# Kernel optimization log

Measured on AMD Instinct MI355X. Metric: run time of the kernel, lower is better.

The kernel has to match this reference:

```python
import jax, jax.numpy as jnp
import numpy as np

B, TV, TS, D = 16, 256, 32, 512


def setup_inputs() -> dict:
    key = jax.random.key(0)
    ks = jax.random.split(key, 8)
    return {
        "video_feature": jax.random.normal(ks[0], (B, TV, D), dtype=jnp.float32),
        "video_mask": jnp.ones((B, TV), dtype=jnp.float32),
        "sentence_feature": jax.random.normal(ks[1], (B, TS, D), dtype=jnp.float32),
        "sentence_mask": jnp.ones((B, TS), dtype=jnp.float32),
        "w1": jax.random.normal(ks[2], (D, D), dtype=jnp.float32) * (1.0 / np.sqrt(D)),
        "b1": jax.random.normal(ks[3], (D,), dtype=jnp.float32) * 0.02,
        "w2": jax.random.normal(ks[4], (D, D), dtype=jnp.float32) * (1.0 / np.sqrt(D)),
        "wt": jax.random.normal(ks[5], (D,), dtype=jnp.float32) * (1.0 / np.sqrt(D)),
    }


def reference(video_feature, video_mask, sentence_feature, sentence_mask, w1, b1, w2, wt):
    # tmp1: [B, Tv, D] masked video projection (Linear with bias)
    tmp1 = (jnp.einsum("bvd,ed->bve", video_feature, w1) + b1) * video_mask[:, :, None]
    # tmp2: [B, Ts, D] masked sentence projection (Linear, no bias)
    tmp2 = jnp.einsum("bsd,ed->bse", sentence_feature, w2) * sentence_mask[:, :, None]
    # pairwise mask: [B, Tv, Ts]
    pair_mask = video_mask[:, :, None] * sentence_mask[:, None, :]
    # broadcast-add -> [B, Tv, Ts, D], mask, tanh, reduce with wt -> [B, Tv, Ts]
    tmp = (tmp1[:, :, None, :] + tmp2[:, None, :, :]) * pair_mask[..., None]
    M = jnp.einsum("bvsd,d->bvs", jnp.tanh(tmp), wt)
    return M * pair_mask
```

## Files before the change

### kernel.cpp

```cpp
#include <hip/hip_runtime.h>

#define BB 16
#define TV 256
#define TS 32
#define DD 512

typedef float    floatx4  __attribute__((ext_vector_type(4)));
typedef short    short8   __attribute__((ext_vector_type(8)));
typedef unsigned short ushort8 __attribute__((ext_vector_type(8)));

#define TANH_SCALE 2.885390082f

static __device__ __forceinline__ unsigned short f2bf(float f) {
    unsigned int u = __float_as_uint(f);
    u += 0x7FFFu + ((u >> 16) & 1u);
    return (unsigned short)(u >> 16);
}

__global__ __launch_bounds__(256) void ta_convert(
    const float* __restrict__ video, const float* __restrict__ sent,
    const float* __restrict__ w1,    const float* __restrict__ w2,
    unsigned short* __restrict__ vb, unsigned short* __restrict__ sb,
    unsigned short* __restrict__ w1b, unsigned short* __restrict__ w2b)
{
    const int NV = BB * TV * DD, NS = BB * TS * DD, NW = DD * DD;
    const int base = (blockIdx.x * 256 + threadIdx.x) * 8;
    const float* src; unsigned short* dst; int off;
    if      (base < NV)           { src = video; dst = vb;  off = base; }
    else if (base < NV + NS)      { src = sent;  dst = sb;  off = base - NV; }
    else if (base < NV + NS + NW) { src = w1;    dst = w1b; off = base - NV - NS; }
    else                          { src = w2;    dst = w2b; off = base - NV - NS - NW; }
    const float4 a = *(const float4*)(src + off);
    const float4 b = *(const float4*)(src + off + 4);
    ushort8 o;
    o[0] = f2bf(a.x); o[1] = f2bf(a.y); o[2] = f2bf(a.z); o[3] = f2bf(a.w);
    o[4] = f2bf(b.x); o[5] = f2bf(b.y); o[6] = f2bf(b.z); o[7] = f2bf(b.w);
    *(ushort8*)(dst + off) = o;
}

__global__ __launch_bounds__(256) void ta_mfma_gemm(
    const unsigned short* __restrict__ vb, const unsigned short* __restrict__ w1b,
    const float* __restrict__ b1,          const float* __restrict__ vmask,
    float* __restrict__ tmp1e,
    const unsigned short* __restrict__ sb, const unsigned short* __restrict__ w2b,
    const float* __restrict__ smask,       unsigned short* __restrict__ tmp2h,
    const float* __restrict__ wt,          float* __restrict__ wsum)
{
    const int t = threadIdx.x;

    if (blockIdx.x == 0 && t < 64) {
        float v = 0.f;
        for (int i = t; i < DD; i += 64) v += wt[i];
        for (int off = 32; off; off >>= 1) v += __shfl_down(v, off);
        if (t == 0) wsum[0] = v;
    }

    const bool g2 = (blockIdx.x >= 512);
    const int bid = g2 ? (int)blockIdx.x - 512 : (int)blockIdx.x;
    const unsigned short* __restrict__ A = g2 ? sb    : vb;
    const unsigned short* __restrict__ W = g2 ? w2b   : w1b;
    const float* __restrict__ rm         = g2 ? smask : vmask;
    const int m0 = (g2 ? (bid & 7)  : (bid & 63)) * 64;
    const int n0 = (g2 ? (bid >> 3) : (bid >> 6)) * 64;

    __shared__ unsigned short As[2][4096];
    __shared__ unsigned short Bs[2][4096];

    const int lane = t & 63;
    const int wid  = t >> 6;
    const int wm   = wid >> 1, wn = wid & 1;
    const int lr   = lane & 15, kg = lane >> 4;

    const int r0 = t >> 3,          g0c = (t & 7) ^ (r0 & 7);
    const int r1 = (t + 256) >> 3,  g1c = (t & 7) ^ (r1 & 7);
    const unsigned short* a0p = A + (size_t)(m0 + r0) * DD + g0c * 8;
    const unsigned short* a1p = A + (size_t)(m0 + r1) * DD + g1c * 8;
    const unsigned short* w0p = W + (size_t)(n0 + r0) * DD + g0c * 8;
    const unsigned short* w1p = W + (size_t)(n0 + r1) * DD + g1c * 8;
    const int l0 = t * 8;
    const int l1 = (t + 256) * 8;

#define TA_STAGE(buf, koff) do {                                               \
    __builtin_amdgcn_global_load_lds(                                          \
        (const __attribute__((address_space(1))) void*)(a0p + (koff)),         \
        (__attribute__((address_space(3))) void*)&As[buf][l0], 16, 0, 0);      \
    __builtin_amdgcn_global_load_lds(                                          \
        (const __attribute__((address_space(1))) void*)(a1p + (koff)),         \
        (__attribute__((address_space(3))) void*)&As[buf][l1], 16, 0, 0);      \
    __builtin_amdgcn_global_load_lds(                                          \
        (const __attribute__((address_space(1))) void*)(w0p + (koff)),         \
        (__attribute__((address_space(3))) void*)&Bs[buf][l0], 16, 0, 0);      \
    __builtin_amdgcn_global_load_lds(                                          \
        (const __attribute__((address_space(1))) void*)(w1p + (koff)),         \
        (__attribute__((address_space(3))) void*)&Bs[buf][l1], 16, 0, 0);      \
  } while (0)

    floatx4 acc[2][2] = {};

    const int ml0 = wm * 32 + lr, ml1 = ml0 + 16;
    const int nl0 = wn * 32 + lr, nl1 = nl0 + 16;
    const int sa0 = ml0 * 64, sa1 = ml1 * 64;
    const int sb0 = nl0 * 64, sb1 = nl1 * 64;
    const int xa = ml0 & 7, xb = nl0 & 7;

    TA_STAGE(0, 0);
    __syncthreads();

    int cur = 0;
    for (int step = 0; step < 8; ++step) {
        if (step < 7) TA_STAGE(cur ^ 1, (step + 1) * 64);
#pragma unroll
        for (int kk = 0; kk < 2; ++kk) {
            const int kc = kk * 4 + kg;
            short8 a0 = *(const short8*)&As[cur][sa0 + ((kc ^ xa) << 3)];
            short8 a1 = *(const short8*)&As[cur][sa1 + ((kc ^ xa) << 3)];
            short8 b0 = *(const short8*)&Bs[cur][sb0 + ((kc ^ xb) << 3)];
            short8 b1 = *(const short8*)&Bs[cur][sb1 + ((kc ^ xb) << 3)];
            acc[0][0] = __builtin_amdgcn_mfma_f32_16x16x32_bf16(a0, b0, acc[0][0], 0, 0, 0);
            acc[0][1] = __builtin_amdgcn_mfma_f32_16x16x32_bf16(a0, b1, acc[0][1], 0, 0, 0);
            acc[1][0] = __builtin_amdgcn_mfma_f32_16x16x32_bf16(a1, b0, acc[1][0], 0, 0, 0);
            acc[1][1] = __builtin_amdgcn_mfma_f32_16x16x32_bf16(a1, b1, acc[1][1], 0, 0, 0);
        }
        __syncthreads();
        cur ^= 1;
    }
#undef TA_STAGE

#pragma unroll
    for (int fm = 0; fm < 2; ++fm)
#pragma unroll
        for (int fn = 0; fn < 2; ++fn)
#pragma unroll
            for (int r = 0; r < 4; ++r) {
                const int m = m0 + wm * 32 + fm * 16 + kg * 4 + r;
                const int n = n0 + wn * 32 + fn * 16 + lr;
                const float mk = rm[m] * TANH_SCALE;
                float z = g2 ? (acc[fm][fn][r] * mk)
                             : (acc[fm][fn][r] + b1[n]) * mk;
                z = fminf(fmaxf(z, -30.f), 30.f);
                const float e = __builtin_amdgcn_exp2f(z);
                if (!g2) {
                    tmp1e[(size_t)m * DD + n] = e;
                } else {
                    tmp2h[(size_t)(m >> 5) * 16384 + (size_t)(n >> 1) * 64
                          + (m & 31) * 2 + (n & 1)] = f2bf(e);
                }
            }
}

__global__ __launch_bounds__(512, 4) void ta_tanh_main(
    const float* __restrict__ tmp1e,
    const unsigned short* __restrict__ tmp2h,
    const float* __restrict__ wt,
    const float* __restrict__ wsum,
    const float* __restrict__ vmask,
    const float* __restrict__ smask,
    float* __restrict__ out)
{
    __shared__ unsigned int t2u[8192];
    __shared__ float e1s[8 * DD];
    __shared__ float part[1024];

    const int t  = threadIdx.x;
    const int b  = blockIdx.x >> 5;
    const int v0 = (blockIdx.x & 31) << 3;

    {
        const ushort8* src = (const ushort8*)(tmp2h + (size_t)b * 16384);
        ushort8* dst = (ushort8*)t2u;
#pragma unroll
        for (int i = 0; i < 4; ++i) dst[t + 512 * i] = src[t + 512 * i];
#pragma unroll
        for (int i = 0; i < 2; ++i) {
            const int c = t + 512 * i;
            const int row = c >> 7, col = (c & 127) << 2;
            *(float4*)&e1s[row * DD + col] =
                *(const float4*)&tmp1e[(size_t)(b * TV + v0 + row) * DD + col];
        }
    }
    __syncthreads();

    const int s  = t & 31;
    const int vi = (t >> 5) & 3;
    const int q  = t >> 7;

    const float* __restrict__ e1lo = e1s + vi * DD + q * 128;
    const float* __restrict__ e1hi = e1s + (vi + 4) * DD + q * 128;
    const float* __restrict__ wtp  = wt + q * 128;
    const int ubase = q * 2048 + s;

    floatx4 alo = {0.f, 0.f, 0.f, 0.f};
    floatx4 ahi = {0.f, 0.f, 0.f, 0.f};
#pragma unroll 4
    for (int i = 0; i < 16; ++i) {
        const int ub = ubase + i * 128;
        const unsigned u0 = t2u[ub];
        const unsigned u1 = t2u[ub + 32];
        const unsigned u2 = t2u[ub + 64];
        const unsigned u3 = t2u[ub + 96];
        floatx4 xl0 = *(const floatx4*)(e1lo + i * 8);
        floatx4 xl1 = *(const floatx4*)(e1lo + i * 8 + 4);
        floatx4 xh0 = *(const floatx4*)(e1hi + i * 8);
        floatx4 xh1 = *(const floatx4*)(e1hi + i * 8 + 4);
        floatx4 wa  = *(const floatx4*)(wtp + i * 8);
        floatx4 wb  = *(const floatx4*)(wtp + i * 8 + 4);
        float e2[8] = {
            __uint_as_float(u0 << 16), __uint_as_float(u0 & 0xffff0000u),
            __uint_as_float(u1 << 16), __uint_as_float(u1 & 0xffff0000u),
            __uint_as_float(u2 << 16), __uint_as_float(u2 & 0xffff0000u),
            __uint_as_float(u3 << 16), __uint_as_float(u3 & 0xffff0000u)
        };
#pragma unroll
        for (int j = 0; j < 4; ++j) {
            const float dlo = fmaf(xl0[j], e2[j], 1.f);
            const float dhi = fmaf(xh0[j], e2[j], 1.f);
            const float inv = __builtin_amdgcn_rcpf(dlo * dhi);
            alo[j] = fmaf(wa[j], dhi * inv, alo[j]);
            ahi[j] = fmaf(wa[j], dlo * inv, ahi[j]);
        }
#pragma unroll
        for (int j = 0; j < 4; ++j) {
            const float dlo = fmaf(xl1[j], e2[j + 4], 1.f);
            const float dhi = fmaf(xh1[j], e2[j + 4], 1.f);
            const float inv = __builtin_amdgcn_rcpf(dlo * dhi);
            alo[j] = fmaf(wb[j], dhi * inv, alo[j]);
            ahi[j] = fmaf(wb[j], dlo * inv, ahi[j]);
        }
    }

    part[vi * 128 + s * 4 + q]       = (alo[0] + alo[1]) + (alo[2] + alo[3]);
    part[(vi + 4) * 128 + s * 4 + q] = (ahi[0] + ahi[1]) + (ahi[2] + ahi[3]);
    __syncthreads();

    if (t < 256) {
        const int sv = t >> 5, s2 = t & 31;
        const float4 p4 = *(const float4*)&part[sv * 128 + s2 * 4];
        const float sum = (p4.x + p4.y) + (p4.z + p4.w);
        const int v = v0 + sv;
        const float pm = vmask[b * TV + v] * smask[b * TS + s2];
        out[((size_t)b * TV + v) * TS + s2] = pm * (wsum[0] - 2.f * sum);
    }
}

extern "C" void kernel_launch(void* const* d_in, const int* in_sizes, int n_in,
                              void* d_out, int out_size, void* d_ws, size_t ws_size,
                              hipStream_t stream)
{
    const float* video = (const float*)d_in[0];
    const float* vmask = (const float*)d_in[1];
    const float* sent  = (const float*)d_in[2];
    const float* smask = (const float*)d_in[3];
    const float* w1    = (const float*)d_in[4];
    const float* b1    = (const float*)d_in[5];
    const float* w2    = (const float*)d_in[6];
    const float* wt    = (const float*)d_in[7];
    float* out = (float*)d_out;

    const size_t NV = (size_t)BB * TV * DD, NS = (size_t)BB * TS * DD, NW = (size_t)DD * DD;

    float* tmp1e         = (float*)d_ws;
    unsigned short* tmp2h = (unsigned short*)(tmp1e + NV);
    unsigned short* vb   = tmp2h + NS;
    unsigned short* sb   = vb + NV;
    unsigned short* w1b  = sb + NS;
    unsigned short* w2b  = w1b + NW;
    float* wsum          = (float*)(w2b + NW);

    const int total8 = (int)((NV + NS + 2 * NW) / 8);
    ta_convert<<<dim3(total8 / 256), dim3(256), 0, stream>>>(
        video, sent, w1, w2, vb, sb, w1b, w2b);
    ta_mfma_gemm<<<dim3(512 + 64), dim3(256), 0, stream>>>(
        vb, w1b, b1, vmask, tmp1e, sb, w2b, smask, tmp2h, wt, wsum);
    ta_tanh_main<<<dim3(BB * (TV / 8)), dim3(512), 0, stream>>>(
        tmp1e, tmp2h, wt, wsum, vmask, smask, out);
}
```

Baseline: 36.44 us.

## Store tmp1 exp as bf16 and retile tanh kernel into smaller sentence-split blocks

The video projection's exp output is now stored as bf16 instead of fp32, which halves that intermediate's write and read traffic. The sentence intermediate is re-laid out in two halves of 16 sentences. The main tanh kernel now runs 256-thread blocks, each covering 4 video rows and 16 sentences, giving four times as many blocks. Video values are read straight from global memory rather than staged in shared memory. Risks are lower precision on tmp1 and more redundant global loads of the e1 rows across the two sentence halves.

```diff
diff --git a/kernel.cpp b/kernel.cpp
--- a/kernel.cpp
+++ b/kernel.cpp
@@ -41,7 +41,7 @@
 __global__ __launch_bounds__(256) void ta_mfma_gemm(
     const unsigned short* __restrict__ vb, const unsigned short* __restrict__ w1b,
     const float* __restrict__ b1,          const float* __restrict__ vmask,
-    float* __restrict__ tmp1e,
+    unsigned short* __restrict__ tmp1h,
     const unsigned short* __restrict__ sb, const unsigned short* __restrict__ w2b,
     const float* __restrict__ smask,       unsigned short* __restrict__ tmp2h,
     const float* __restrict__ wt,          float* __restrict__ wsum)
@@ -140,16 +140,17 @@
                 z = fminf(fmaxf(z, -30.f), 30.f);
                 const float e = __builtin_amdgcn_exp2f(z);
                 if (!g2) {
-                    tmp1e[(size_t)m * DD + n] = e;
+                    tmp1h[(size_t)m * DD + n] = f2bf(e);
                 } else {
-                    tmp2h[(size_t)(m >> 5) * 16384 + (size_t)(n >> 1) * 64
-                          + (m & 31) * 2 + (n & 1)] = f2bf(e);
+                    const int bb = m >> 5, ss = m & 31;
+                    tmp2h[(size_t)bb * 16384 + (size_t)(ss >> 4) * 8192
+                          + (size_t)(n >> 1) * 32 + (ss & 15) * 2 + (n & 1)] = f2bf(e);
                 }
             }
 }
 
-__global__ __launch_bounds__(512, 4) void ta_tanh_main(
-    const float* __restrict__ tmp1e,
+__global__ __launch_bounds__(256) void ta_tanh_main(
+    const unsigned short* __restrict__ tmp1h,
     const unsigned short* __restrict__ tmp2h,
     const float* __restrict__ wt,
     const float* __restrict__ wsum,
@@ -157,54 +158,48 @@
     const float* __restrict__ smask,
     float* __restrict__ out)
 {
-    __shared__ unsigned int t2u[8192];
-    __shared__ float e1s[8 * DD];
-    __shared__ float part[1024];
-
-    const int t  = threadIdx.x;
-    const int b  = blockIdx.x >> 5;
-    const int v0 = (blockIdx.x & 31) << 3;
+    __shared__ unsigned int e2u[4096];
+    __shared__ float part[512];
+
+    const int t   = threadIdx.x;
+    const int bid = blockIdx.x;
+    const int b   = bid >> 7;
+    const int vt  = (bid >> 1) & 63;
+    const int sh  = bid & 1;
+    const int v0  = vt << 2;
 
     {
-        const ushort8* src = (const ushort8*)(tmp2h + (size_t)b * 16384);
-        ushort8* dst = (ushort8*)t2u;
-#pragma unroll
-        for (int i = 0; i < 4; ++i) dst[t + 512 * i] = src[t + 512 * i];
-#pragma unroll
-        for (int i = 0; i < 2; ++i) {
-            const int c = t + 512 * i;
-            const int row = c >> 7, col = (c & 127) << 2;
-            *(float4*)&e1s[row * DD + col] =
-                *(const float4*)&tmp1e[(size_t)(b * TV + v0 + row) * DD + col];
-        }
+        const ushort8* src = (const ushort8*)(tmp2h + (size_t)b * 16384 + sh * 8192);
+        ushort8* dst = (ushort8*)e2u;
+#pragma unroll
+        for (int i = 0; i < 4; ++i) dst[t + 256 * i] = src[t + 256 * i];
     }
     __syncthreads();
 
-    const int s  = t & 31;
-    const int vi = (t >> 5) & 3;
-    const int q  = t >> 7;
-
-    const float* __restrict__ e1lo = e1s + vi * DD + q * 128;
-    const float* __restrict__ e1hi = e1s + (vi + 4) * DD + q * 128;
-    const float* __restrict__ wtp  = wt + q * 128;
-    const int ubase = q * 2048 + s;
+    const int s  = t & 15;
+    const int vi = (t >> 4) & 1;
+    const int q  = t >> 5;
+
+    const unsigned short* __restrict__ e1lo =
+        tmp1h + (size_t)(b * TV + v0 + vi) * DD + q * 64;
+    const unsigned short* __restrict__ e1hi = e1lo + 2 * DD;
+    const float* __restrict__ wtp = wt + q * 64;
+    const int ubase = (q * 32) * 16 + s;
 
     floatx4 alo = {0.f, 0.f, 0.f, 0.f};
     floatx4 ahi = {0.f, 0.f, 0.f, 0.f};
-#pragma unroll 4
-    for (int i = 0; i < 16; ++i) {
-        const int ub = ubase + i * 128;
-        const unsigned u0 = t2u[ub];
-        const unsigned u1 = t2u[ub + 32];
-        const unsigned u2 = t2u[ub + 64];
-        const unsigned u3 = t2u[ub + 96];
-        floatx4 xl0 = *(const floatx4*)(e1lo + i * 8);
-        floatx4 xl1 = *(const floatx4*)(e1lo + i * 8 + 4);
-        floatx4 xh0 = *(const floatx4*)(e1hi + i * 8);
-        floatx4 xh1 = *(const floatx4*)(e1hi + i * 8 + 4);
-        floatx4 wa  = *(const floatx4*)(wtp + i * 8);
-        floatx4 wb  = *(const floatx4*)(wtp + i * 8 + 4);
-        float e2[8] = {
+#pragma unroll 2
+    for (int i = 0; i < 8; ++i) {
+        const int ub = ubase + i * 64;
+        const unsigned u0 = e2u[ub];
+        const unsigned u1 = e2u[ub + 16];
+        const unsigned u2 = e2u[ub + 32];
+        const unsigned u3 = e2u[ub + 48];
+        ushort8 l8 = *(const ushort8*)(e1lo + i * 8);
+        ushort8 h8 = *(const ushort8*)(e1hi + i * 8);
+        floatx4 wa = *(const floatx4*)(wtp + i * 8);
+        floatx4 wb = *(const floatx4*)(wtp + i * 8 + 4);
+        const float e2v[8] = {
             __uint_as_float(u0 << 16), __uint_as_float(u0 & 0xffff0000u),
             __uint_as_float(u1 << 16), __uint_as_float(u1 & 0xffff0000u),
             __uint_as_float(u2 << 16), __uint_as_float(u2 & 0xffff0000u),
@@ -212,33 +207,40 @@
         };
 #pragma unroll
         for (int j = 0; j < 4; ++j) {
-            const float dlo = fmaf(xl0[j], e2[j], 1.f);
-            const float dhi = fmaf(xh0[j], e2[j], 1.f);
+            const float xl = __uint_as_float((unsigned)l8[j] << 16);
+            const float xh = __uint_as_float((unsigned)h8[j] << 16);
+            const float dlo = fmaf(xl, e2v[j], 1.f);
+            const float dhi = fmaf(xh, e2v[j], 1.f);
             const float inv = __builtin_amdgcn_rcpf(dlo * dhi);
             alo[j] = fmaf(wa[j], dhi * inv, alo[j]);
             ahi[j] = fmaf(wa[j], dlo * inv, ahi[j]);
         }
 #pragma unroll
         for (int j = 0; j < 4; ++j) {
-            const float dlo = fmaf(xl1[j], e2[j + 4], 1.f);
-            const float dhi = fmaf(xh1[j], e2[j + 4], 1.f);
+            const float xl = __uint_as_float((unsigned)l8[j + 4] << 16);
+            const float xh = __uint_as_float((unsigned)h8[j + 4] << 16);
+            const float dlo = fmaf(xl, e2v[j + 4], 1.f);
+            const float dhi = fmaf(xh, e2v[j + 4], 1.f);
             const float inv = __builtin_amdgcn_rcpf(dlo * dhi);
             alo[j] = fmaf(wb[j], dhi * inv, alo[j]);
             ahi[j] = fmaf(wb[j], dlo * inv, ahi[j]);
         }
     }
 
-    part[vi * 128 + s * 4 + q]       = (alo[0] + alo[1]) + (alo[2] + alo[3]);
-    part[(vi + 4) * 128 + s * 4 + q] = (ahi[0] + ahi[1]) + (ahi[2] + ahi[3]);
+    part[(vi    ) * 128 + s * 8 + q] = (alo[0] + alo[1]) + (alo[2] + alo[3]);
+    part[(vi + 2) * 128 + s * 8 + q] = (ahi[0] + ahi[1]) + (ahi[2] + ahi[3]);
     __syncthreads();
 
-    if (t < 256) {
-        const int sv = t >> 5, s2 = t & 31;
-        const float4 p4 = *(const float4*)&part[sv * 128 + s2 * 4];
-        const float sum = (p4.x + p4.y) + (p4.z + p4.w);
-        const int v = v0 + sv;
-        const float pm = vmask[b * TV + v] * smask[b * TS + s2];
-        out[((size_t)b * TV + v) * TS + s2] = pm * (wsum[0] - 2.f * sum);
+    if (t < 64) {
+        const int vrow = t >> 4, s2 = t & 15;
+        const floatx4 p0 = *(const floatx4*)&part[vrow * 128 + s2 * 8];
+        const floatx4 p1 = *(const floatx4*)&part[vrow * 128 + s2 * 8 + 4];
+        const float sum = ((p0[0] + p0[1]) + (p0[2] + p0[3]))
+                        + ((p1[0] + p1[1]) + (p1[2] + p1[3]));
+        const int v  = v0 + vrow;
+        const int sg = sh * 16 + s2;
+        const float pm = vmask[b * TV + v] * smask[b * TS + sg];
+        out[((size_t)b * TV + v) * TS + sg] = pm * (wsum[0] - 2.f * sum);
     }
 }
 
@@ -258,19 +260,19 @@
 
     const size_t NV = (size_t)BB * TV * DD, NS = (size_t)BB * TS * DD, NW = (size_t)DD * DD;
 
-    float* tmp1e         = (float*)d_ws;
-    unsigned short* tmp2h = (unsigned short*)(tmp1e + NV);
-    unsigned short* vb   = tmp2h + NS;
-    unsigned short* sb   = vb + NV;
-    unsigned short* w1b  = sb + NS;
-    unsigned short* w2b  = w1b + NW;
-    float* wsum          = (float*)(w2b + NW);
+    unsigned short* tmp1h = (unsigned short*)d_ws;
+    unsigned short* tmp2h = tmp1h + NV;
+    unsigned short* vb    = tmp2h + NS;
+    unsigned short* sb    = vb + NV;
+    unsigned short* w1b   = sb + NS;
+    unsigned short* w2b   = w1b + NW;
+    float* wsum           = (float*)(w2b + NW);
 
     const int total8 = (int)((NV + NS + 2 * NW) / 8);
     ta_convert<<<dim3(total8 / 256), dim3(256), 0, stream>>>(
         video, sent, w1, w2, vb, sb, w1b, w2b);
     ta_mfma_gemm<<<dim3(512 + 64), dim3(256), 0, stream>>>(
-        vb, w1b, b1, vmask, tmp1e, sb, w2b, smask, tmp2h, wt, wsum);
-    ta_tanh_main<<<dim3(BB * (TV / 8)), dim3(512), 0, stream>>>(
-        tmp1e, tmp2h, wt, wsum, vmask, smask, out);
-}
+        vb, w1b, b1, vmask, tmp1h, sb, w2b, smask, tmp2h, wt, wsum);
+    ta_tanh_main<<<dim3(BB * (TV / 4) * 2), dim3(256), 0, stream>>>(
+        tmp1h, tmp2h, wt, wsum, vmask, smask, out);
+}
```

Result: no change. 35.76 us (-1.9%).
